# Performance work log

Measured on AMD Instinct MI355X. Metric: run time of the kernel, lower is better.

## Reference

```python
import jax, jax.numpy as jnp
import numpy as np

V, D = 1_000_000, 128
N0, N1, N2 = 1_048_576, 131_072, 16_384
E0, E1, EP = 1_048_576, 131_072, 16_384


def setup_inputs() -> dict:
    key = jax.random.key(0)
    ks = jax.random.split(key, 20)
    inp = {
        'emb': jax.random.normal(ks[0], (V, D), jnp.float32) * 0.1,
        'bias': jnp.zeros((V, 1), jnp.float32),
        'nids': jax.random.randint(ks[1], (N0,), 0, V),
        'src0': jax.random.randint(ks[2], (E0,), 0, N0),
        'dst0': jax.random.randint(ks[3], (E0,), 0, N1),
        'w0': jax.random.uniform(ks[4], (E0,), jnp.float32),
        'src1': jax.random.randint(ks[5], (E1,), 0, N1),
        'dst1': jax.random.randint(ks[6], (E1,), 0, N2),
        'w1': jax.random.uniform(ks[7], (E1,), jnp.float32),
        'pos_src': jax.random.randint(ks[8], (EP,), 0, N2),
        'pos_dst': jax.random.randint(ks[9], (EP,), 0, N2),
        'neg_src': jax.random.randint(ks[10], (EP,), 0, N2),
        'neg_dst': jax.random.randint(ks[11], (EP,), 0, N2),
        'Q0w': jax.random.normal(ks[12], (D, D), jnp.float32) / np.sqrt(D),
        'Q0b': jnp.zeros((D,), jnp.float32),
        'W0w': jax.random.normal(ks[13], (2 * D, D), jnp.float32) / np.sqrt(2 * D),
        'W0b': jnp.zeros((D,), jnp.float32),
        'Q1w': jax.random.normal(ks[14], (D, D), jnp.float32) / np.sqrt(D),
        'Q1b': jnp.zeros((D,), jnp.float32),
        'W1w': jax.random.normal(ks[15], (2 * D, D), jnp.float32) / np.sqrt(2 * D),
        'W1b': jnp.zeros((D,), jnp.float32),
    }
    return inp


def _sage_conv(h_src, h_dst, src, dst, w, Qw, Qb, Ww, Wb, n_dst):
    # n = relu(Q h_src); m = sum_e w_e * n[src_e] per dst; ws = sum_e w_e per dst
    n = jax.nn.relu(h_src @ Qw + Qb)                                   # [N_src, H]
    m = jax.ops.segment_sum(n[src] * w[:, None], dst, num_segments=n_dst)
    ws = jnp.clip(jax.ops.segment_sum(w, dst, num_segments=n_dst), 1.0, None)[:, None]
    z = jax.nn.relu(jnp.concatenate([m / ws, h_dst], axis=1) @ Ww + Wb)
    zn = jnp.linalg.norm(z, axis=1, keepdims=True)
    return z / jnp.where(zn == 0, 1.0, zn)


def _pair_score(h, bias_nid, src, dst):
    # u_dot_v + bias_src + bias_dst  -> [E, 1]
    s = jnp.sum(h[src] * h[dst], axis=1, keepdims=True)
    return s + bias_nid[src] + bias_nid[dst]


def reference(emb, bias, nids, src0, dst0, w0, src1, dst1, w1,
              pos_src, pos_dst, neg_src, neg_dst,
              Q0w, Q0b, W0w, W0b, Q1w, Q1b, W1w, W1b):
    h = emb[nids]                                                      # [N0, D]
    h1 = _sage_conv(h, h[:N1], src0, dst0, w0, Q0w, Q0b, W0w, W0b, N1)  # [N1, D]
    h2 = _sage_conv(h1, h1[:N2], src1, dst1, w1, Q1w, Q1b, W1w, W1b, N2)  # [N2, D]
    h_item = emb[nids[:N2]] + h2                                       # [N2, D]
    bias_nid = bias[nids[:N2]]                                         # [N2, 1]
    pos = _pair_score(h_item, bias_nid, pos_src, pos_dst)
    neg = _pair_score(h_item, bias_nid, neg_src, neg_dst)
    return jax.nn.relu(neg - pos + 1.0)                                # [EP, 1]
```

## Files before the change

kernel.cpp:

```cpp
#include <hip/hip_runtime.h>
#include <stdint.h>

#define V_SZ   1000000
#define N0_SZ  1048576
#define N1_SZ  131072
#define N2_SZ  16384
#define E0_SZ  1048576
#define E1_SZ  131072
#define EP_SZ  16384

typedef short bf16x8 __attribute__((ext_vector_type(8)));
typedef float f32x4  __attribute__((ext_vector_type(4)));

__device__ __forceinline__ unsigned short f2bf(float f) {
  union { float f; unsigned u; } v; v.f = f;
  unsigned r = v.u + 0x7FFFu + ((v.u >> 16) & 1u);
  return (unsigned short)(r >> 16);
}
__device__ __forceinline__ float bf2f(unsigned short h) {
  union { unsigned u; float f; } v; v.u = ((unsigned)h) << 16;
  return v.f;
}
__device__ __forceinline__ unsigned pack2bf(float a, float b) {
  return ((unsigned)f2bf(b) << 16) | (unsigned)f2bf(a);
}

__global__ __launch_bounds__(256) void prepw_all_k(
    const float* __restrict__ Q0w, const float* __restrict__ W0w,
    const float* __restrict__ Q1w, const float* __restrict__ W1w,
    unsigned short* __restrict__ Q0T, unsigned short* __restrict__ W0T,
    unsigned short* __restrict__ Q1T, unsigned short* __restrict__ W1T) {
  int t = blockIdx.x * 256 + threadIdx.x;
  const float* W; unsigned short* WT; int K; int base;
  if (t < 16384)      { W = Q0w; WT = Q0T; K = 128; base = 0; }
  else if (t < 49152) { W = W0w; WT = W0T; K = 256; base = 16384; }
  else if (t < 65536) { W = Q1w; WT = Q1T; K = 128; base = 49152; }
  else                { W = W1w; WT = W1T; K = 256; base = 65536; }
  int u = t - base;
  int n = u & 127, k = u >> 7;
  WT[(size_t)n * K + k] = f2bf(W[u]);
}

__global__ __launch_bounds__(256) void hist_all_k(const int* __restrict__ dst0,
                                                  const int* __restrict__ dst1,
                                                  int* __restrict__ counts) {
  int e = blockIdx.x * 256 + threadIdx.x;
  if (e < E0_SZ) atomicAdd(&counts[dst0[e]], 1);
  else if (e < E0_SZ + E1_SZ) atomicAdd(&counts[N1_SZ + dst1[e - E0_SZ]], 1);
}

__global__ __launch_bounds__(256) void scan_bsums_k(const int* __restrict__ counts,
                                                    int* __restrict__ bsums) {
  __shared__ int red[256];
  int base = blockIdx.x * 1024, t = threadIdx.x;
  int s = 0;
  #pragma unroll
  for (int i = 0; i < 4; i++) s += counts[base + t * 4 + i];
  red[t] = s;
  __syncthreads();
  for (int st = 128; st > 0; st >>= 1) {
    if (t < st) red[t] += red[t + st];
    __syncthreads();
  }
  if (t == 0) bsums[blockIdx.x] = red[0];
}

__global__ __launch_bounds__(256) void scan_top2_k(int* __restrict__ bsums,
                                                   int* __restrict__ offs0_last,
                                                   int* __restrict__ offs1_last) {
  __shared__ int lds[256];
  int b = blockIdx.x, t = threadIdx.x;
  int nb = (b == 0) ? 128 : 16;
  int off = (b == 0) ? 0 : 128;
  int v = (t < nb) ? bsums[off + t] : 0;
  lds[t] = v;
  __syncthreads();
  for (int st = 1; st < 256; st <<= 1) {
    int x = (t >= st) ? lds[t - st] : 0;
    __syncthreads();
    lds[t] += x;
    __syncthreads();
  }
  if (t < nb) bsums[off + t] = lds[t] - v;
  if (t == nb - 1) *((b == 0) ? offs0_last : offs1_last) = lds[t];
}

__global__ __launch_bounds__(256) void scan_final_k(const int* __restrict__ counts,
                                                    const int* __restrict__ bsums,
                                                    int* __restrict__ offs0,
                                                    int* __restrict__ offs1) {
  __shared__ int tsum[256];
  int b = blockIdx.x, t = threadIdx.x;
  int base = b * 1024;
  int v0 = counts[base + t * 4 + 0], v1 = counts[base + t * 4 + 1];
  int v2 = counts[base + t * 4 + 2], v3 = counts[base + t * 4 + 3];
  int s = v0 + v1 + v2 + v3;
  tsum[t] = s;
  __syncthreads();
  for (int st = 1; st < 256; st <<= 1) {
    int x = (t >= st) ? tsum[t - st] : 0;
    __syncthreads();
    tsum[t] += x;
    __syncthreads();
  }
  int pre = bsums[b] + tsum[t] - s;
  int* op = (b < 128) ? (offs0 + base) : (offs1 + base - N1_SZ);
  op[t * 4 + 0] = pre;
  op[t * 4 + 1] = pre + v0;
  op[t * 4 + 2] = pre + v0 + v1;
  op[t * 4 + 3] = pre + v0 + v1 + v2;
}

__global__ __launch_bounds__(256) void scatter_all_k(
    const int* __restrict__ src0, const int* __restrict__ dst0, const float* __restrict__ w0,
    const int* __restrict__ src1, const int* __restrict__ dst1, const float* __restrict__ w1,
    const int* __restrict__ offs0, const int* __restrict__ offs1,
    int* __restrict__ cursor,
    int* __restrict__ srcs_s0, float* __restrict__ ws_s0,
    int* __restrict__ srcs_s1, float* __restrict__ ws_s1) {
  int e = blockIdx.x * 256 + threadIdx.x;
  if (e < E0_SZ) {
    int d = dst0[e];
    int p = offs0[d] + atomicAdd(&cursor[d], 1);
    srcs_s0[p] = src0[e];
    ws_s0[p] = w0[e];
  } else if (e < E0_SZ + E1_SZ) {
    int ee = e - E0_SZ;
    int d = dst1[ee];
    int p = offs1[d] + atomicAdd(&cursor[N1_SZ + d], 1);
    srcs_s1[p] = src1[ee];
    ws_s1[p] = w1[ee];
  }
}

#define AM_GATHER 0
#define AM_BF16   1
#define EPI_BF16        0
#define EPI_NORM        1
#define EPI_NORM_ADDEMB 2

template <int KCHUNKS, int AM0, int AM1, int EPI>
__global__ __launch_bounds__(256) void gemm_k(const void* __restrict__ asrc0,
                                              const void* __restrict__ asrc1,
                                              const int* __restrict__ ids,
                                              const unsigned short* __restrict__ BT,
                                              const float* __restrict__ biasv,
                                              void* __restrict__ outp,
                                              const float* __restrict__ emb) {
  __shared__ unsigned short lA[64][136];
  __shared__ unsigned short lB[128][136];
  const int tid = threadIdx.x;
  const int lane = tid & 63;
  const int wid = tid >> 6;
  const int rowbase = blockIdx.x * 64;
  const int Ktot = KCHUNKS * 128;

  f32x4 acc[8];
  #pragma unroll
  for (int i = 0; i < 8; i++) acc[i] = (f32x4){0.f, 0.f, 0.f, 0.f};

  for (int c = 0; c < KCHUNKS; ++c) {
    if (c) __syncthreads();
    const int am = (c == 0) ? AM0 : AM1;
    const void* asrc = (c == 0) ? asrc0 : asrc1;
    if (am == AM_GATHER) {
      const float* fsrc = (const float*)asrc;
      #pragma unroll
      for (int i = 0; i < 8; i++) {
        int f = i * 256 + tid;
        int r = f >> 5, c4 = f & 31;
        const float* rp = fsrc + (size_t)ids[rowbase + r] * 128;
        float4 v = *(const float4*)(rp + c4 * 4);
        uint2 pk;
        pk.x = pack2bf(v.x, v.y);
        pk.y = pack2bf(v.z, v.w);
        *(uint2*)(&lA[r][c4 * 4]) = pk;
      }
    } else {
      const unsigned short* bsrc = (const unsigned short*)asrc;
      #pragma unroll
      for (int i = 0; i < 4; i++) {
        int f = i * 256 + tid;
        int r = f >> 4, c8 = f & 15;
        uint4 v = *(const uint4*)(bsrc + (size_t)(rowbase + r) * 128 + c8 * 8);
        *(uint4*)(&lA[r][c8 * 8]) = v;
      }
    }
    {
      const unsigned short* bp = BT + c * 128;
      #pragma unroll
      for (int i = 0; i < 8; i++) {
        int f = i * 256 + tid;
        int n = f >> 4, c8 = f & 15;
        uint4 v = *(const uint4*)(bp + (size_t)n * Ktot + c8 * 8);
        *(uint4*)(&lB[n][c8 * 8]) = v;
      }
    }
    __syncthreads();

    const int mr = wid * 16 + (lane & 15);
    const int kq = (lane >> 4) * 8;
    #pragma unroll
    for (int kk = 0; kk < 128; kk += 32) {
      bf16x8 af = *(const bf16x8*)(&lA[mr][kk + kq]);
      #pragma unroll
      for (int nt = 0; nt < 8; ++nt) {
        bf16x8 bfr = *(const bf16x8*)(&lB[nt * 16 + (lane & 15)][kk + kq]);
        acc[nt] = __builtin_amdgcn_mfma_f32_16x16x32_bf16(af, bfr, acc[nt], 0, 0, 0);
      }
    }
  }

  const int crow = wid * 16 + ((lane >> 4) << 2);
  float vreg[8][4];
  #pragma unroll
  for (int nt = 0; nt < 8; ++nt) {
    int col = nt * 16 + (lane & 15);
    float b = biasv[col];
    #pragma unroll
    for (int r = 0; r < 4; ++r) {
      float v = acc[nt][r] + b;
      vreg[nt][r] = v > 0.f ? v : 0.f;
    }
  }
  if (EPI == EPI_BF16) {
    unsigned short* op = (unsigned short*)outp;
    #pragma unroll
    for (int nt = 0; nt < 8; ++nt) {
      int col = nt * 16 + (lane & 15);
      #pragma unroll
      for (int r = 0; r < 4; ++r)
        op[(size_t)(rowbase + crow + r) * 128 + col] = f2bf(vreg[nt][r]);
    }
  } else {
    float ss[4] = {0.f, 0.f, 0.f, 0.f};
    #pragma unroll
    for (int nt = 0; nt < 8; ++nt)
      #pragma unroll
      for (int r = 0; r < 4; ++r) ss[r] += vreg[nt][r] * vreg[nt][r];
    #pragma unroll
    for (int r = 0; r < 4; ++r) {
      ss[r] += __shfl_xor(ss[r], 1);
      ss[r] += __shfl_xor(ss[r], 2);
      ss[r] += __shfl_xor(ss[r], 4);
      ss[r] += __shfl_xor(ss[r], 8);
    }
    float sc[4];
    #pragma unroll
    for (int r = 0; r < 4; ++r) sc[r] = ss[r] > 0.f ? rsqrtf(ss[r]) : 1.0f;
    if (EPI == EPI_NORM) {
      unsigned short* op = (unsigned short*)outp;
      #pragma unroll
      for (int nt = 0; nt < 8; ++nt) {
        int col = nt * 16 + (lane & 15);
        #pragma unroll
        for (int r = 0; r < 4; ++r)
          op[(size_t)(rowbase + crow + r) * 128 + col] = f2bf(vreg[nt][r] * sc[r]);
      }
    } else {
      float* op = (float*)outp;
      #pragma unroll
      for (int nt = 0; nt < 8; ++nt) {
        int col = nt * 16 + (lane & 15);
        #pragma unroll
        for (int r = 0; r < 4; ++r) {
          int row = rowbase + crow + r;
          op[(size_t)row * 128 + col] =
              vreg[nt][r] * sc[r] + emb[(size_t)ids[row] * 128 + col];
        }
      }
    }
  }
}

__global__ __launch_bounds__(256) void agg_k(const unsigned short* __restrict__ nsrc,
                                             const int* __restrict__ offs,
                                             const int* __restrict__ srcs_s,
                                             const float* __restrict__ ws_s,
                                             unsigned short* __restrict__ aout, int ndst) {
  int wid = threadIdx.x >> 6, lane = threadIdx.x & 63;
  int d = blockIdx.x * 4 + wid;
  if (d >= ndst) return;
  int beg = offs[d], end = offs[d + 1];
  float ax = 0.f, ay = 0.f, wsum = 0.f;
  for (int base = beg; base < end; base += 64) {
    int cnt = min(64, end - base);
    int sv = 0; float wv = 0.f;
    if (lane < cnt) { sv = srcs_s[base + lane]; wv = ws_s[base + lane]; }
    int j = 0;
    for (; j + 4 <= cnt; j += 4) {
      int s0 = __shfl(sv, j),     s1 = __shfl(sv, j + 1);
      int s2 = __shfl(sv, j + 2), s3 = __shfl(sv, j + 3);
      float w0 = __shfl(wv, j),     w1 = __shfl(wv, j + 1);
      float w2 = __shfl(wv, j + 2), w3 = __shfl(wv, j + 3);
      unsigned u0 = *(const unsigned*)(nsrc + (size_t)s0 * 128 + lane * 2);
      unsigned u1 = *(const unsigned*)(nsrc + (size_t)s1 * 128 + lane * 2);
      unsigned u2 = *(const unsigned*)(nsrc + (size_t)s2 * 128 + lane * 2);
      unsigned u3 = *(const unsigned*)(nsrc + (size_t)s3 * 128 + lane * 2);
      ax += w0 * bf2f((unsigned short)(u0 & 0xffff));
      ay += w0 * bf2f((unsigned short)(u0 >> 16));
      ax += w1 * bf2f((unsigned short)(u1 & 0xffff));
      ay += w1 * bf2f((unsigned short)(u1 >> 16));
      ax += w2 * bf2f((unsigned short)(u2 & 0xffff));
      ay += w2 * bf2f((unsigned short)(u2 >> 16));
      ax += w3 * bf2f((unsigned short)(u3 & 0xffff));
      ay += w3 * bf2f((unsigned short)(u3 >> 16));
      wsum += w0 + w1 + w2 + w3;
    }
    for (; j < cnt; ++j) {
      int s = __shfl(sv, j);
      float w = __shfl(wv, j);
      unsigned u = *(const unsigned*)(nsrc + (size_t)s * 128 + lane * 2);
      ax += w * bf2f((unsigned short)(u & 0xffff));
      ay += w * bf2f((unsigned short)(u >> 16));
      wsum += w;
    }
  }
  float inv = 1.0f / fmaxf(wsum, 1.0f);
  unsigned o = ((unsigned)f2bf(ay * inv) << 16) | (unsigned)f2bf(ax * inv);
  *(unsigned*)(aout + (size_t)d * 128 + lane * 2) = o;
}

__global__ __launch_bounds__(256) void score_k(const float* __restrict__ hitem,
                                               const float* __restrict__ bias,
                                               const int* __restrict__ nids,
                                               const int* __restrict__ ps,
                                               const int* __restrict__ pd,
                                               const int* __restrict__ ns,
                                               const int* __restrict__ nd,
                                               float* __restrict__ out) {
  int wid = threadIdx.x >> 6, lane = threadIdx.x & 63;
  int e = blockIdx.x * 4 + wid;
  if (e >= EP_SZ) return;
  int a = ps[e], b = pd[e], c = ns[e], d = nd[e];
  float2 va = ((const float2*)(hitem + (size_t)a * 128))[lane];
  float2 vb = ((const float2*)(hitem + (size_t)b * 128))[lane];
  float2 vc = ((const float2*)(hitem + (size_t)c * 128))[lane];
  float2 vd = ((const float2*)(hitem + (size_t)d * 128))[lane];
  float dp = va.x * vb.x + va.y * vb.y;
  float dn = vc.x * vd.x + vc.y * vd.y;
  #pragma unroll
  for (int m = 1; m < 64; m <<= 1) {
    dp += __shfl_xor(dp, m);
    dn += __shfl_xor(dn, m);
  }
  if (lane == 0) {
    float sp = dp + bias[nids[a]] + bias[nids[b]];
    float sn = dn + bias[nids[c]] + bias[nids[d]];
    out[e] = fmaxf(sn - sp + 1.0f, 0.0f);
  }
}

extern "C" void kernel_launch(void* const* d_in, const int* in_sizes, int n_in,
                              void* d_out, int out_size, void* d_ws, size_t ws_size,
                              hipStream_t stream) {
  const float* emb  = (const float*)d_in[0];
  const float* bias = (const float*)d_in[1];
  const int* nids   = (const int*)d_in[2];
  const int* src0   = (const int*)d_in[3];
  const int* dst0   = (const int*)d_in[4];
  const float* w0   = (const float*)d_in[5];
  const int* src1   = (const int*)d_in[6];
  const int* dst1   = (const int*)d_in[7];
  const float* w1   = (const float*)d_in[8];
  const int* pos_src = (const int*)d_in[9];
  const int* pos_dst = (const int*)d_in[10];
  const int* neg_src = (const int*)d_in[11];
  const int* neg_dst = (const int*)d_in[12];
  const float* Q0w = (const float*)d_in[13];
  const float* Q0b = (const float*)d_in[14];
  const float* W0w = (const float*)d_in[15];
  const float* W0b = (const float*)d_in[16];
  const float* Q1w = (const float*)d_in[17];
  const float* Q1b = (const float*)d_in[18];
  const float* W1w = (const float*)d_in[19];
  const float* W1b = (const float*)d_in[20];
  float* out = (float*)d_out;

  char* ws = (char*)d_ws;
  size_t p = 0;
  auto carve = [&](size_t sz) { void* r = ws + p; p = (p + sz + 255) & ~(size_t)255; return r; };

  unsigned short* n0 = (unsigned short*)carve((size_t)N0_SZ * 128 * 2);
  unsigned short* h1    = (unsigned short*)(ws + 0);
  unsigned short* n1    = (unsigned short*)(ws + 33554432);
  unsigned short* a1    = (unsigned short*)(ws + 67108864);
  float*          hitem = (float*)(ws + 71303168);

  unsigned short* a0  = (unsigned short*)carve((size_t)N1_SZ * 128 * 2);
  unsigned short* Q0T = (unsigned short*)carve(128 * 128 * 2);
  unsigned short* W0T = (unsigned short*)carve(256 * 128 * 2);
  unsigned short* Q1T = (unsigned short*)carve(128 * 128 * 2);
  unsigned short* W1T = (unsigned short*)carve(256 * 128 * 2);
  int* cnt_all = (int*)carve((size_t)(N1_SZ + N2_SZ) * 2 * 4);
  int* counts  = cnt_all;
  int* cursor  = cnt_all + (N1_SZ + N2_SZ);
  int*   offs0   = (int*)carve((N1_SZ + 1) * 4);
  int*   offs1   = (int*)carve((N2_SZ + 1) * 4);
  int*   srcs_s0 = (int*)carve(E0_SZ * 4);
  float* ws_s0   = (float*)carve(E0_SZ * 4);
  int*   srcs_s1 = (int*)carve(E1_SZ * 4);
  float* ws_s1   = (float*)carve(E1_SZ * 4);
  int*   bsums   = (int*)carve(160 * 4);
  (void)ws_size; (void)in_sizes; (void)n_in; (void)out_size;

  hipMemsetAsync(cnt_all, 0, (size_t)(N1_SZ + N2_SZ) * 2 * 4, stream);

  prepw_all_k<<<384, 256, 0, stream>>>(Q0w, W0w, Q1w, W1w, Q0T, W0T, Q1T, W1T);

  hist_all_k<<<(E0_SZ + E1_SZ) / 256, 256, 0, stream>>>(dst0, dst1, counts);
  scan_bsums_k<<<(N1_SZ + N2_SZ) / 1024, 256, 0, stream>>>(counts, bsums);
  scan_top2_k<<<2, 256, 0, stream>>>(bsums, offs0 + N1_SZ, offs1 + N2_SZ);
  scan_final_k<<<(N1_SZ + N2_SZ) / 1024, 256, 0, stream>>>(counts, bsums, offs0, offs1);
  scatter_all_k<<<(E0_SZ + E1_SZ) / 256, 256, 0, stream>>>(
      src0, dst0, w0, src1, dst1, w1, offs0, offs1, cursor,
      srcs_s0, ws_s0, srcs_s1, ws_s1);

  gemm_k<1, AM_GATHER, AM_GATHER, EPI_BF16>
      <<<N0_SZ / 64, 256, 0, stream>>>(emb, nullptr, nids, Q0T, Q0b, n0, nullptr);
  agg_k<<<N1_SZ / 4, 256, 0, stream>>>(n0, offs0, srcs_s0, ws_s0, a0, N1_SZ);
  gemm_k<2, AM_BF16, AM_GATHER, EPI_NORM>
      <<<N1_SZ / 64, 256, 0, stream>>>(a0, emb, nids, W0T, W0b, h1, nullptr);
  gemm_k<1, AM_BF16, AM_BF16, EPI_BF16>
      <<<N1_SZ / 64, 256, 0, stream>>>(h1, nullptr, nullptr, Q1T, Q1b, n1, nullptr);
  agg_k<<<N2_SZ / 4, 256, 0, stream>>>(n1, offs1, srcs_s1, ws_s1, a1, N2_SZ);
  gemm_k<2, AM_BF16, AM_BF16, EPI_NORM_ADDEMB>
      <<<N2_SZ / 64, 256, 0, stream>>>(a1, h1, nids, W1T, W1b, hitem, emb);

  score_k<<<EP_SZ / 4, 256, 0, stream>>>(hitem, bias, nids, pos_src, pos_dst,
                                         neg_src, neg_dst, out);
}
```

Before: 1.044 ms.

## Fuse Q projection into edge aggregation, computing messages per edge

Replaces the separate full-node Q GEMM plus gather-aggregate with a fused kernel. For each block of 64 destinations it gathers source features per edge into LDS, applies the Q projection with MFMA and ReLU, then reduces weighted messages per destination. This removes the materialised n0/n1 tensors, including the 1M-row layer-0 GEMM over all source nodes. In exchange it recomputes the projection once per edge rather than once per node; E0 equals N0, so the FLOPs are similar. Edge src and weight are also packed into a single int2 array so both arrive in one load.

Measured after the change: 1.197 ms. 1.15x slower.

```diff
diff --git a/kernel.cpp b/kernel.cpp
--- a/kernel.cpp
+++ b/kernel.cpp
@@ -116,20 +116,17 @@
     const int* __restrict__ src1, const int* __restrict__ dst1, const float* __restrict__ w1,
     const int* __restrict__ offs0, const int* __restrict__ offs1,
     int* __restrict__ cursor,
-    int* __restrict__ srcs_s0, float* __restrict__ ws_s0,
-    int* __restrict__ srcs_s1, float* __restrict__ ws_s1) {
+    int2* __restrict__ esw0, int2* __restrict__ esw1) {
   int e = blockIdx.x * 256 + threadIdx.x;
   if (e < E0_SZ) {
     int d = dst0[e];
     int p = offs0[d] + atomicAdd(&cursor[d], 1);
-    srcs_s0[p] = src0[e];
-    ws_s0[p] = w0[e];
+    esw0[p] = make_int2(src0[e], __float_as_int(w0[e]));
   } else if (e < E0_SZ + E1_SZ) {
     int ee = e - E0_SZ;
     int d = dst1[ee];
     int p = offs1[d] + atomicAdd(&cursor[N1_SZ + d], 1);
-    srcs_s1[p] = src1[ee];
-    ws_s1[p] = w1[ee];
+    esw1[p] = make_int2(src1[ee], __float_as_int(w1[ee]));
   }
 }
 
@@ -273,52 +270,127 @@
   }
 }
 
-__global__ __launch_bounds__(256) void agg_k(const unsigned short* __restrict__ nsrc,
-                                             const int* __restrict__ offs,
-                                             const int* __restrict__ srcs_s,
-                                             const float* __restrict__ ws_s,
-                                             unsigned short* __restrict__ aout, int ndst) {
-  int wid = threadIdx.x >> 6, lane = threadIdx.x & 63;
-  int d = blockIdx.x * 4 + wid;
-  if (d >= ndst) return;
-  int beg = offs[d], end = offs[d + 1];
-  float ax = 0.f, ay = 0.f, wsum = 0.f;
-  for (int base = beg; base < end; base += 64) {
-    int cnt = min(64, end - base);
-    int sv = 0; float wv = 0.f;
-    if (lane < cnt) { sv = srcs_s[base + lane]; wv = ws_s[base + lane]; }
-    int j = 0;
-    for (; j + 4 <= cnt; j += 4) {
-      int s0 = __shfl(sv, j),     s1 = __shfl(sv, j + 1);
-      int s2 = __shfl(sv, j + 2), s3 = __shfl(sv, j + 3);
-      float w0 = __shfl(wv, j),     w1 = __shfl(wv, j + 1);
-      float w2 = __shfl(wv, j + 2), w3 = __shfl(wv, j + 3);
-      unsigned u0 = *(const unsigned*)(nsrc + (size_t)s0 * 128 + lane * 2);
-      unsigned u1 = *(const unsigned*)(nsrc + (size_t)s1 * 128 + lane * 2);
-      unsigned u2 = *(const unsigned*)(nsrc + (size_t)s2 * 128 + lane * 2);
-      unsigned u3 = *(const unsigned*)(nsrc + (size_t)s3 * 128 + lane * 2);
-      ax += w0 * bf2f((unsigned short)(u0 & 0xffff));
-      ay += w0 * bf2f((unsigned short)(u0 >> 16));
-      ax += w1 * bf2f((unsigned short)(u1 & 0xffff));
-      ay += w1 * bf2f((unsigned short)(u1 >> 16));
-      ax += w2 * bf2f((unsigned short)(u2 & 0xffff));
-      ay += w2 * bf2f((unsigned short)(u2 >> 16));
-      ax += w3 * bf2f((unsigned short)(u3 & 0xffff));
-      ay += w3 * bf2f((unsigned short)(u3 >> 16));
-      wsum += w0 + w1 + w2 + w3;
-    }
-    for (; j < cnt; ++j) {
-      int s = __shfl(sv, j);
-      float w = __shfl(wv, j);
-      unsigned u = *(const unsigned*)(nsrc + (size_t)s * 128 + lane * 2);
-      ax += w * bf2f((unsigned short)(u & 0xffff));
-      ay += w * bf2f((unsigned short)(u >> 16));
-      wsum += w;
-    }
-  }
-  float inv = 1.0f / fmaxf(wsum, 1.0f);
-  unsigned o = ((unsigned)f2bf(ay * inv) << 16) | (unsigned)f2bf(ax * inv);
-  *(unsigned*)(aout + (size_t)d * 128 + lane * 2) = o;
+template <int LAYER>
+__global__ __launch_bounds__(256) void qagg_k(
+    const float* __restrict__ embf,
+    const unsigned short* __restrict__ hsrc,
+    const int* __restrict__ nids,
+    const int* __restrict__ offs,
+    const int2* __restrict__ esw,
+    const unsigned short* __restrict__ BT,
+    const float* __restrict__ biasv,
+    unsigned short* __restrict__ aout) {
+  __shared__ unsigned short lA[64][136];
+  __shared__ unsigned short lB[128][136];
+  __shared__ float lw[64];
+  __shared__ int loffs[65];
+  const int tid = threadIdx.x;
+  const int lane = tid & 63;
+  const int wid = tid >> 6;
+  const int d0 = blockIdx.x * 64;
+
+  #pragma unroll
+  for (int i = 0; i < 8; i++) {
+    int f = i * 256 + tid;
+    int n = f >> 4, c8 = f & 15;
+    uint4 v = *(const uint4*)(BT + (size_t)n * 128 + c8 * 8);
+    *(uint4*)(&lB[n][c8 * 8]) = v;
+  }
+  if (tid < 65) loffs[tid] = offs[d0 + tid];
+  const int ebeg = offs[d0];
+  const int eend = offs[d0 + 64];
+
+  const int mr = wid * 16 + (lane & 15);
+  const int kq = (lane >> 4) * 8;
+  const int crow = wid * 16 + ((lane >> 4) << 2);
+
+  float bv[8];
+  #pragma unroll
+  for (int nt = 0; nt < 8; ++nt) bv[nt] = biasv[nt * 16 + (lane & 15)];
+
+  float accD[16][2];
+  float wsum[16];
+  #pragma unroll
+  for (int i = 0; i < 16; ++i) { accD[i][0] = 0.f; accD[i][1] = 0.f; wsum[i] = 0.f; }
+
+  for (int base = ebeg; base < eend; base += 64) {
+    const int nslots = min(64, eend - base);
+    if (tid < 64) lw[tid] = (tid < nslots) ? __int_as_float(esw[base + tid].y) : 0.f;
+    if (LAYER == 0) {
+      #pragma unroll
+      for (int i = 0; i < 8; i++) {
+        int f = i * 256 + tid;
+        int r = f >> 5, c4 = f & 31;
+        if (r < nslots) {
+          int s = esw[base + r].x;
+          const float* rp = embf + (size_t)nids[s] * 128;
+          float4 v = *(const float4*)(rp + c4 * 4);
+          uint2 pk;
+          pk.x = pack2bf(v.x, v.y);
+          pk.y = pack2bf(v.z, v.w);
+          *(uint2*)(&lA[r][c4 * 4]) = pk;
+        }
+      }
+    } else {
+      #pragma unroll
+      for (int i = 0; i < 4; i++) {
+        int f = i * 256 + tid;
+        int r = f >> 4, c8 = f & 15;
+        if (r < nslots) {
+          int s = esw[base + r].x;
+          uint4 v = *(const uint4*)(hsrc + (size_t)s * 128 + c8 * 8);
+          *(uint4*)(&lA[r][c8 * 8]) = v;
+        }
+      }
+    }
+    __syncthreads();
+
+    f32x4 acc[8];
+    #pragma unroll
+    for (int i = 0; i < 8; i++) acc[i] = (f32x4){0.f, 0.f, 0.f, 0.f};
+    #pragma unroll
+    for (int kk = 0; kk < 128; kk += 32) {
+      bf16x8 af = *(const bf16x8*)(&lA[mr][kk + kq]);
+      #pragma unroll
+      for (int nt = 0; nt < 8; ++nt) {
+        bf16x8 bfr = *(const bf16x8*)(&lB[nt * 16 + (lane & 15)][kk + kq]);
+        acc[nt] = __builtin_amdgcn_mfma_f32_16x16x32_bf16(af, bfr, acc[nt], 0, 0, 0);
+      }
+    }
+    #pragma unroll
+    for (int nt = 0; nt < 8; ++nt) {
+      int col = nt * 16 + (lane & 15);
+      #pragma unroll
+      for (int r = 0; r < 4; ++r) {
+        float v = acc[nt][r] + bv[nt];
+        lA[crow + r][col] = f2bf(v > 0.f ? v : 0.f);
+      }
+    }
+    __syncthreads();
+
+    #pragma unroll
+    for (int dd = 0; dd < 16; ++dd) {
+      const int d = wid * 16 + dd;
+      int rb = loffs[d] - base;     rb = rb > 0 ? rb : 0;
+      int re = loffs[d + 1] - base; re = re < nslots ? re : nslots;
+      for (int r = rb; r < re; ++r) {
+        float w = lw[r];
+        unsigned u = *(const unsigned*)(&lA[r][lane * 2]);
+        accD[dd][0] += w * bf2f((unsigned short)(u & 0xffffu));
+        accD[dd][1] += w * bf2f((unsigned short)(u >> 16));
+        wsum[dd] += w;
+      }
+    }
+    __syncthreads();
+  }
+
+  #pragma unroll
+  for (int dd = 0; dd < 16; ++dd) {
+    const int d = d0 + wid * 16 + dd;
+    float inv = 1.0f / fmaxf(wsum[dd], 1.0f);
+    unsigned o = pack2bf(accD[dd][0] * inv, accD[dd][1] * inv);
+    *(unsigned*)(aout + (size_t)d * 128 + lane * 2) = o;
+  }
 }
 
 __global__ __launch_bounds__(256) void score_k(const float* __restrict__ hitem,
@@ -381,13 +453,10 @@
   size_t p = 0;
   auto carve = [&](size_t sz) { void* r = ws + p; p = (p + sz + 255) & ~(size_t)255; return r; };
 
-  unsigned short* n0 = (unsigned short*)carve((size_t)N0_SZ * 128 * 2);
-  unsigned short* h1    = (unsigned short*)(ws + 0);
-  unsigned short* n1    = (unsigned short*)(ws + 33554432);
-  unsigned short* a1    = (unsigned short*)(ws + 67108864);
-  float*          hitem = (float*)(ws + 71303168);
-
-  unsigned short* a0  = (unsigned short*)carve((size_t)N1_SZ * 128 * 2);
+  unsigned short* a0    = (unsigned short*)carve((size_t)N1_SZ * 128 * 2);
+  unsigned short* h1    = (unsigned short*)carve((size_t)N1_SZ * 128 * 2);
+  unsigned short* a1    = (unsigned short*)carve((size_t)N2_SZ * 128 * 2);
+  float*          hitem = (float*)carve((size_t)N2_SZ * 128 * 4);
   unsigned short* Q0T = (unsigned short*)carve(128 * 128 * 2);
   unsigned short* W0T = (unsigned short*)carve(256 * 128 * 2);
   unsigned short* Q1T = (unsigned short*)carve(128 * 128 * 2);
@@ -395,13 +464,11 @@
   int* cnt_all = (int*)carve((size_t)(N1_SZ + N2_SZ) * 2 * 4);
   int* counts  = cnt_all;
   int* cursor  = cnt_all + (N1_SZ + N2_SZ);
-  int*   offs0   = (int*)carve((N1_SZ + 1) * 4);
-  int*   offs1   = (int*)carve((N2_SZ + 1) * 4);
-  int*   srcs_s0 = (int*)carve(E0_SZ * 4);
-  float* ws_s0   = (float*)carve(E0_SZ * 4);
-  int*   srcs_s1 = (int*)carve(E1_SZ * 4);
-  float* ws_s1   = (float*)carve(E1_SZ * 4);
-  int*   bsums   = (int*)carve(160 * 4);
+  int*  offs0 = (int*)carve((N1_SZ + 1) * 4);
+  int*  offs1 = (int*)carve((N2_SZ + 1) * 4);
+  int2* esw0  = (int2*)carve((size_t)E0_SZ * 8);
+  int2* esw1  = (int2*)carve((size_t)E1_SZ * 8);
+  int*  bsums = (int*)carve(160 * 4);
   (void)ws_size; (void)in_sizes; (void)n_in; (void)out_size;
 
   hipMemsetAsync(cnt_all, 0, (size_t)(N1_SZ + N2_SZ) * 2 * 4, stream);
@@ -413,17 +480,14 @@
   scan_top2_k<<<2, 256, 0, stream>>>(bsums, offs0 + N1_SZ, offs1 + N2_SZ);
   scan_final_k<<<(N1_SZ + N2_SZ) / 1024, 256, 0, stream>>>(counts, bsums, offs0, offs1);
   scatter_all_k<<<(E0_SZ + E1_SZ) / 256, 256, 0, stream>>>(
-      src0, dst0, w0, src1, dst1, w1, offs0, offs1, cursor,
-      srcs_s0, ws_s0, srcs_s1, ws_s1);
-
-  gemm_k<1, AM_GATHER, AM_GATHER, EPI_BF16>
-      <<<N0_SZ / 64, 256, 0, stream>>>(emb, nullptr, nids, Q0T, Q0b, n0, nullptr);
-  agg_k<<<N1_SZ / 4, 256, 0, stream>>>(n0, offs0, srcs_s0, ws_s0, a0, N1_SZ);
+      src0, dst0, w0, src1, dst1, w1, offs0, offs1, cursor, esw0, esw1);
+
+  qagg_k<0><<<N1_SZ / 64, 256, 0, stream>>>(emb, nullptr, nids, offs0, esw0,
+                                            Q0T, Q0b, a0);
   gemm_k<2, AM_BF16, AM_GATHER, EPI_NORM>
       <<<N1_SZ / 64, 256, 0, stream>>>(a0, emb, nids, W0T, W0b, h1, nullptr);
-  gemm_k<1, AM_BF16, AM_BF16, EPI_BF16>
-      <<<N1_SZ / 64, 256, 0, stream>>>(h1, nullptr, nullptr, Q1T, Q1b, n1, nullptr);
-  agg_k<<<N2_SZ / 4, 256, 0, stream>>>(n1, offs1, srcs_s1, ws_s1, a1, N2_SZ);
+  qagg_k<1><<<N2_SZ / 64, 256, 0, stream>>>(nullptr, h1, nullptr, offs1, esw1,
+                                            Q1T, Q1b, a1);
   gemm_k<2, AM_BF16, AM_BF16, EPI_NORM_ADDEMB>
       <<<N2_SZ / 64, 256, 0, stream>>>(a1, h1, nids, W1T, W1b, hitem, emb);
 
```
